# Kernel tuning notes

Measured on AMD Instinct MI355X. Metric: run time of the kernel, lower is better.

Reference implementation:

```python
import jax, jax.numpy as jnp
import numpy as np

EMBED_DIM = 1024
NUM_HEADS = 16
D_K = EMBED_DIM // NUM_HEADS  # 64 quantum wires per head


def setup_inputs() -> dict:
    key = jax.random.key(0)
    k1, k2, k3 = jax.random.split(key, 3)
    x = jax.random.normal(k1, (8, 2048, EMBED_DIM), dtype=jnp.float32)
    # single shared projection weight (source creates ONE nn.Linear used for q,k,v and out)
    W = jax.random.normal(k2, (EMBED_DIM, EMBED_DIM), dtype=jnp.float32) * 0.02
    # trainable RY angles, one per wire, shared across tokens and heads
    theta = jax.random.normal(k3, (D_K,), dtype=jnp.float32)
    return {"x": x, "W": W, "theta": theta}


def _quantum_project(h, theta):
    # h: [B, S, E] -> per-head wires [B, S, H, d_k]
    # Circuit per wire i: |0> -> RX(h_i) -> RY(theta_i) -> <Z>
    # Product state closed form: <Z> = cos(theta_i) * cos(h_i)
    B, S, E = h.shape
    hw = h.reshape(B, S, NUM_HEADS, D_K)
    return jnp.cos(theta) * jnp.cos(hw)  # [B, S, H, d_k]


def reference(x, W, theta):
    # one Linear (no bias) shared by q, k, v -> identical projections
    proj = x @ W.T  # [B, S, E]
    qq = _quantum_project(proj, theta)  # == k_q == v_q, [B, S, H, d_k]
    # scores attend heads-vs-heads per token (faithful to source matmul on dims -2,-1)
    scores = jnp.einsum('bshd,bsgd->bshg', qq, qq) / np.sqrt(D_K).astype(np.float32)
    attn = jax.nn.softmax(scores, axis=-1)  # dropout omitted (eval)
    out = jnp.einsum('bshg,bsgd->bshd', attn, qq)  # [B, S, H, d_k]
    B, S = x.shape[0], x.shape[1]
    out = out.reshape(B, S, EMBED_DIM) @ W.T  # output projection with same shared linear
    return out
```

## Files before the change

### kernel.cpp

```cpp
#include <hip/hip_runtime.h>
#include <hip/hip_bf16.h>
#include <stdint.h>

#define NB    8
#define NS    2048
#define NE    1024
#define NH    16
#define NDK   64
#define MTOK  (NB*NS)

typedef __attribute__((ext_vector_type(8))) short bf16x8;
typedef __attribute__((ext_vector_type(4))) float f32x4;

__device__ __forceinline__ ushort f2bf(float f) {
  uint32_t u = __float_as_uint(f);
  u += 0x7FFFu + ((u >> 16) & 1u);
  return (ushort)(u >> 16);
}

__device__ __forceinline__ void gload16(const void* g, void* l) {
  __builtin_amdgcn_global_load_lds(
      (const __attribute__((address_space(1))) void*)g,
      (__attribute__((address_space(3))) void*)l, 16, 0, 0);
}

__global__ __launch_bounds__(256) void cvt_bf16(const float* __restrict__ in,
                                                ushort* __restrict__ out, int n4) {
  int stride = gridDim.x * blockDim.x;
  for (int j = blockIdx.x * blockDim.x + threadIdx.x; j < n4; j += stride) {
    float4 v = ((const float4*)in)[j];
    ushort4 o;
    o.x = f2bf(v.x); o.y = f2bf(v.y); o.z = f2bf(v.z); o.w = f2bf(v.w);
    ((ushort4*)out)[j] = o;
  }
}

#define GM 256
#define GN 256
#define GK 64
#define KC 1024
#define NKT (KC / GK)

template<int EPI>
__global__ __launch_bounds__(512, 2) void gemm256(const ushort* __restrict__ A,
                                                  const ushort* __restrict__ Bm,
                                                  float* __restrict__ Cf,
                                                  ushort* __restrict__ Cq,
                                                  const float* __restrict__ theta,
                                                  int M, int N, int K) {
  __shared__ ushort As[2][GM * GK];
  __shared__ ushort Bs[2][GN * GK];

  const int tid  = threadIdx.x;
  const int wid  = tid >> 6;
  const int lane = tid & 63;
  const int wr   = wid >> 2;
  const int wc   = wid & 3;
  const int fr   = lane & 15;
  const int ks   = lane >> 4;

  int b  = blockIdx.x;
  int wg = ((b & 7) << 5) | (b >> 3);
  int br = wg >> 2, bc = wg & 3;

  const ushort* Abase = A  + (size_t)(br * GM) * KC;
  const ushort* Bbase = Bm + (size_t)(bc * GN) * KC;

  const int srow = lane >> 3;
  const int sch8 = ((lane & 7) ^ srow) * 8;

  const int sA0 = ((0 + ks) ^ (fr & 7)) * 8;
  const int sA1 = ((4 + ks) ^ (fr & 7)) * 8;

  f32x4 zero = {0.f, 0.f, 0.f, 0.f};
  f32x4 acc[8][4];
#pragma unroll
  for (int mi = 0; mi < 8; ++mi)
#pragma unroll
    for (int ni = 0; ni < 4; ++ni) acc[mi][ni] = zero;

  auto stA = [&](int buf, int mh, int kt) {
#pragma unroll
    for (int j = 0; j < 2; ++j) {
      int rl = mh * 128 + j * 64 + wid * 8;
      gload16(Abase + (size_t)(rl + srow) * KC + kt * GK + sch8,
              &As[buf][rl * GK]);
    }
  };
  auto stB = [&](int buf, int mh, int kt) {
#pragma unroll
    for (int j = 0; j < 2; ++j) {
      int rl = mh * 128 + j * 64 + wid * 8;
      gload16(Bbase + (size_t)(rl + srow) * KC + kt * GK + sch8,
              &Bs[buf][rl * GK]);
    }
  };

  stB(0, 0, 0); stB(0, 1, 0); stA(0, 0, 0); stA(0, 1, 0);
  asm volatile("s_waitcnt vmcnt(2)" ::: "memory");
  __builtin_amdgcn_s_barrier();

  int cur = 0;
  for (int t = 0; t < NKT; ++t) {
    const ushort* Ac = As[cur];
    const ushort* Bc = Bs[cur];
    const int nb = cur ^ 1;
    const bool pf = (t + 1 < NKT);
    bf16x8 af[4], bv[4];

#pragma unroll
    for (int mi = 0; mi < 4; ++mi)
      af[mi] = *(const bf16x8*)&Ac[(mi * 32 + wr * 16 + fr) * GK + sA0];
#pragma unroll
    for (int ni = 0; ni < 4; ++ni)
      bv[ni] = *(const bf16x8*)&Bc[(ni * 64 + wc * 16 + fr) * GK + sA0];
    if (pf) { stB(nb, 0, t + 1); stB(nb, 1, t + 1); stA(nb, 0, t + 1); stA(nb, 1, t + 1); }
    __builtin_amdgcn_sched_barrier(0);
    __builtin_amdgcn_s_setprio(1);
#pragma unroll
    for (int mi = 0; mi < 4; ++mi)
#pragma unroll
      for (int ni = 0; ni < 4; ++ni)
        acc[mi][ni] = __builtin_amdgcn_mfma_f32_16x16x32_bf16(af[mi], bv[ni], acc[mi][ni], 0, 0, 0);
    __builtin_amdgcn_s_setprio(0);
    __builtin_amdgcn_sched_barrier(0);
    if (pf) asm volatile("s_waitcnt vmcnt(8)" ::: "memory");
    else    asm volatile("s_waitcnt vmcnt(0)" ::: "memory");
    __builtin_amdgcn_s_barrier();

#pragma unroll
    for (int mi = 0; mi < 4; ++mi)
      af[mi] = *(const bf16x8*)&Ac[((mi + 4) * 32 + wr * 16 + fr) * GK + sA0];
    __builtin_amdgcn_sched_barrier(0);
    __builtin_amdgcn_s_setprio(1);
#pragma unroll
    for (int mi = 0; mi < 4; ++mi)
#pragma unroll
      for (int ni = 0; ni < 4; ++ni)
        acc[mi + 4][ni] = __builtin_amdgcn_mfma_f32_16x16x32_bf16(af[mi], bv[ni], acc[mi + 4][ni], 0, 0, 0);
    __builtin_amdgcn_s_setprio(0);
    __builtin_amdgcn_sched_barrier(0);

#pragma unroll
    for (int mi = 0; mi < 4; ++mi)
      af[mi] = *(const bf16x8*)&Ac[(mi * 32 + wr * 16 + fr) * GK + sA1];
#pragma unroll
    for (int ni = 0; ni < 4; ++ni)
      bv[ni] = *(const bf16x8*)&Bc[(ni * 64 + wc * 16 + fr) * GK + sA1];
    __builtin_amdgcn_sched_barrier(0);
    __builtin_amdgcn_s_setprio(1);
#pragma unroll
    for (int mi = 0; mi < 4; ++mi)
#pragma unroll
      for (int ni = 0; ni < 4; ++ni)
        acc[mi][ni] = __builtin_amdgcn_mfma_f32_16x16x32_bf16(af[mi], bv[ni], acc[mi][ni], 0, 0, 0);
    __builtin_amdgcn_s_setprio(0);
    __builtin_amdgcn_sched_barrier(0);

#pragma unroll
    for (int mi = 0; mi < 4; ++mi)
      af[mi] = *(const bf16x8*)&Ac[((mi + 4) * 32 + wr * 16 + fr) * GK + sA1];
    __builtin_amdgcn_sched_barrier(0);
    __builtin_amdgcn_s_setprio(1);
#pragma unroll
    for (int mi = 0; mi < 4; ++mi)
#pragma unroll
      for (int ni = 0; ni < 4; ++ni)
        acc[mi + 4][ni] = __builtin_amdgcn_mfma_f32_16x16x32_bf16(af[mi], bv[ni], acc[mi + 4][ni], 0, 0, 0);
    __builtin_amdgcn_s_setprio(0);
    __builtin_amdgcn_sched_barrier(0);
    if (pf) asm volatile("s_waitcnt vmcnt(2)" ::: "memory");
    __builtin_amdgcn_s_barrier();

    cur ^= 1;
  }

  const int colL = wc * 16 + fr;
  float ct = 0.f;
  if (EPI == 1) ct = __cosf(theta[colL]);
#pragma unroll
  for (int mi = 0; mi < 8; ++mi) {
    int row0 = br * GM + mi * 32 + wr * 16 + ks * 4;
#pragma unroll
    for (int ni = 0; ni < 4; ++ni) {
      size_t cbase = (size_t)row0 * N + bc * GN + ni * 64 + colL;
#pragma unroll
      for (int i = 0; i < 4; ++i) {
        if (EPI == 1)
          Cq[cbase + (size_t)i * N] = f2bf(ct * __cosf(acc[mi][ni][i]));
        else
          Cf[cbase + (size_t)i * N] = acc[mi][ni][i];
      }
    }
  }
}

__global__ __launch_bounds__(256) void attn_quantum(const ushort* __restrict__ qqb,
                                                    ushort* __restrict__ aout) {
  __shared__ ushort T[4][64 * 32];
  int tid = threadIdx.x;
  int wv  = tid >> 6, l = tid & 63;
  size_t tok = (size_t)blockIdx.x * 4 + wv;
  const ushort* src = qqb + tok * NE;
  ushort* Tw = T[wv];

  int h  = l & 15;
  int kb = l >> 4;

  bf16x8 f0 = *(const bf16x8*)(src + h * 64 + kb * 8);
  bf16x8 f1 = *(const bf16x8*)(src + h * 64 + kb * 8 + 32);

#pragma unroll
  for (int jj = 0; jj < 8; ++jj) {
    int d0 = kb * 8 + jj;
    int d1 = d0 + 32;
    Tw[d0 * 32 + (((h >> 3) ^ ((d0 >> 3) & 3)) << 3) + (h & 7)] = (ushort)f0[jj];
    Tw[d1 * 32 + (((h >> 3) ^ ((d1 >> 3) & 3)) << 3) + (h & 7)] = (ushort)f1[jj];
  }

  f32x4 sa = {0.f, 0.f, 0.f, 0.f};
  sa = __builtin_amdgcn_mfma_f32_16x16x32_bf16(f0, f0, sa, 0, 0, 0);
  sa = __builtin_amdgcn_mfma_f32_16x16x32_bf16(f1, f1, sa, 0, 0, 0);

  float s[4];
#pragma unroll
  for (int i = 0; i < 4; ++i) s[i] = sa[i] * 0.125f;

  float mx = fmaxf(fmaxf(s[0], s[1]), fmaxf(s[2], s[3]));
  mx = fmaxf(mx, __shfl_xor(mx, 16));
  mx = fmaxf(mx, __shfl_xor(mx, 32));
  float e[4], sum = 0.f;
#pragma unroll
  for (int i = 0; i < 4; ++i) { e[i] = __expf(s[i] - mx); sum += e[i]; }
  sum += __shfl_xor(sum, 16);
  sum += __shfl_xor(sum, 32);
  float inv = 1.f / sum;
#pragma unroll
  for (int i = 0; i < 4; ++i) e[i] *= inv;

  int s1 = h + (kb & 1) * 32;
  float q1[4], q2[4];
#pragma unroll
  for (int i = 0; i < 4; ++i) {
    q1[i] = __shfl(e[i], s1);
    q2[i] = __shfl(e[i], s1 + 16);
  }
  bool live = (kb < 2);
  bf16x8 pa;
#pragma unroll
  for (int i = 0; i < 4; ++i) {
    pa[i]     = live ? (short)f2bf(q1[i]) : (short)0;
    pa[4 + i] = live ? (short)f2bf(q2[i]) : (short)0;
  }

  __syncthreads();

  f32x4 o[4];
#pragma unroll
  for (int c = 0; c < 4; ++c) {
    int r = c * 16 + h;
    int slot = (kb & 1) ^ ((r >> 3) & 3);
    bf16x8 bfrag = *(const bf16x8*)&Tw[r * 32 + slot * 8];
    f32x4 z = {0.f, 0.f, 0.f, 0.f};
    o[c] = __builtin_amdgcn_mfma_f32_16x16x32_bf16(pa, bfrag, z, 0, 0, 0);
  }

  ushort* dst = aout + tok * NE;
#pragma unroll
  for (int c = 0; c < 4; ++c)
#pragma unroll
    for (int i = 0; i < 4; ++i)
      dst[(kb * 4 + i) * NDK + c * 16 + h] = f2bf(o[c][i]);
}

extern "C" void kernel_launch(void* const* d_in, const int* in_sizes, int n_in,
                              void* d_out, int out_size, void* d_ws, size_t ws_size,
                              hipStream_t stream) {
  const float* x     = (const float*)d_in[0];
  const float* W     = (const float*)d_in[1];
  const float* theta = (const float*)d_in[2];
  float* out = (float*)d_out;

  char* ws = (char*)d_ws;
  ushort* xb   = (ushort*)ws;
  ushort* Wb   = (ushort*)(ws + (size_t)MTOK * NE * 2);
  ushort* qqb  = (ushort*)(ws + (size_t)MTOK * NE * 2 + (size_t)NE * NE * 2);
  ushort* aout = xb;

  cvt_bf16<<<1024, 256, 0, stream>>>(x, xb, MTOK * NE / 4);
  cvt_bf16<<<256, 256, 0, stream>>>(W, Wb, NE * NE / 4);

  int nwg = (MTOK / GM) * (NE / GN);
  gemm256<1><<<nwg, 512, 0, stream>>>(xb, Wb, nullptr, qqb, theta, MTOK, NE, NE);

  attn_quantum<<<MTOK / 4, 256, 0, stream>>>(qqb, aout);

  gemm256<0><<<nwg, 512, 0, stream>>>(aout, Wb, out, nullptr, nullptr, MTOK, NE, NE);
}
```

Measured before the change: 109.9 us.

## Fuse fp32-to-bf16 conversion of x into first projection GEMM

Removes the standalone conversion pass over x and adds a dedicated GEMM that reads fp32 x directly, converts it in registers, and writes bf16 tiles into swizzled LDS with a two-stage register prefetch. The tile is 128x256 with one workgroup per CU, and the cos(theta)*cos(h) epilogue is applied directly. This saves a full write and re-read of the 32MB bf16 copy of x. The trade-off is more global traffic per A tile, since fp32 is twice the bytes, and lower occupancy, which may make the GEMM's latency hiding worse.

```diff
diff --git a/kernel.cpp b/kernel.cpp
--- a/kernel.cpp
+++ b/kernel.cpp
@@ -35,11 +35,178 @@
   }
 }
 
+#define KC 1024
+#define NKT 16
+
+#define QM 128
+#define QN 256
+#define QK 64
+
+#define LOADAQ(kt, AR)                                                        \
+  do {                                                                        \
+    _Pragma("unroll")                                                         \
+    for (int j = 0; j < 4; ++j)                                               \
+      AR[j] = X4[(size_t)(br * QM + ar_r) * 256 + (kt) * 16 + c4 * 4 + j];    \
+  } while (0)
+
+#define WRITEAQ(buf, AR)                                                      \
+  do {                                                                        \
+    bf16x8 v0, v1;                                                            \
+    v0[0] = (short)f2bf(AR[0].x); v0[1] = (short)f2bf(AR[0].y);               \
+    v0[2] = (short)f2bf(AR[0].z); v0[3] = (short)f2bf(AR[0].w);               \
+    v0[4] = (short)f2bf(AR[1].x); v0[5] = (short)f2bf(AR[1].y);               \
+    v0[6] = (short)f2bf(AR[1].z); v0[7] = (short)f2bf(AR[1].w);               \
+    v1[0] = (short)f2bf(AR[2].x); v1[1] = (short)f2bf(AR[2].y);               \
+    v1[2] = (short)f2bf(AR[2].z); v1[3] = (short)f2bf(AR[2].w);               \
+    v1[4] = (short)f2bf(AR[3].x); v1[5] = (short)f2bf(AR[3].y);               \
+    v1[6] = (short)f2bf(AR[3].z); v1[7] = (short)f2bf(AR[3].w);               \
+    *(bf16x8*)&As[buf][ar_r * QK + wrs0] = v0;                                \
+    *(bf16x8*)&As[buf][ar_r * QK + wrs1] = v1;                                \
+  } while (0)
+
+#define QMFMA(MOFF)                                                           \
+  __builtin_amdgcn_sched_barrier(0);                                          \
+  __builtin_amdgcn_s_setprio(1);                                              \
+  _Pragma("unroll")                                                           \
+  for (int mi = 0; mi < 2; ++mi)                                              \
+    _Pragma("unroll")                                                         \
+    for (int ni = 0; ni < 4; ++ni)                                            \
+      acc[mi + (MOFF)][ni] = __builtin_amdgcn_mfma_f32_16x16x32_bf16(         \
+          af[mi], bv[ni], acc[mi + (MOFF)][ni], 0, 0, 0);                     \
+  __builtin_amdgcn_s_setprio(0);                                              \
+  __builtin_amdgcn_sched_barrier(0);
+
+#define BODYQ(T, ARL, ARW)                                                    \
+  {                                                                           \
+    const int t = (T);                                                        \
+    const ushort* Ac = As[cur];                                               \
+    const ushort* Bc = Bs[cur];                                               \
+    const int nb = cur ^ 1;                                                   \
+    const bool pf  = (t + 1 < NKT);                                           \
+    const bool pf2 = (t + 2 < NKT);                                           \
+    bf16x8 af[2], bv[4];                                                      \
+                      \
+    _Pragma("unroll")                                                         \
+    for (int mi = 0; mi < 2; ++mi)                                            \
+      af[mi] = *(const bf16x8*)&Ac[(wr * 64 + mi * 16 + fr) * QK + sA0];      \
+    _Pragma("unroll")                                                         \
+    for (int ni = 0; ni < 4; ++ni)                                            \
+      bv[ni] = *(const bf16x8*)&Bc[(ni * 64 + wc * 16 + fr) * QK + sA0];      \
+    if (pf) { stB(nb, 0, t + 1); stB(nb, 1, t + 1); }                         \
+    if (pf2) LOADAQ(t + 2, ARL);                                              \
+    QMFMA(0)                                                                  \
+                                      \
+    _Pragma("unroll")                                                         \
+    for (int mi = 0; mi < 2; ++mi)                                            \
+      af[mi] = *(const bf16x8*)&Ac[(wr * 64 + (mi + 2) * 16 + fr) * QK + sA0];\
+    QMFMA(2)                                                                  \
+                                                        \
+    _Pragma("unroll")                                                         \
+    for (int mi = 0; mi < 2; ++mi)                                            \
+      af[mi] = *(const bf16x8*)&Ac[(wr * 64 + mi * 16 + fr) * QK + sA1];      \
+    _Pragma("unroll")                                                         \
+    for (int ni = 0; ni < 4; ++ni)                                            \
+      bv[ni] = *(const bf16x8*)&Bc[(ni * 64 + wc * 16 + fr) * QK + sA1];      \
+    QMFMA(0)                                                                  \
+                                  \
+    _Pragma("unroll")                                                         \
+    for (int mi = 0; mi < 2; ++mi)                                            \
+      af[mi] = *(const bf16x8*)&Ac[(wr * 64 + (mi + 2) * 16 + fr) * QK + sA1];\
+    QMFMA(2)                                                                  \
+    if (pf) {                                                                 \
+      if (pf2) asm volatile("s_waitcnt vmcnt(4)" ::: "memory");               \
+      else     asm volatile("s_waitcnt vmcnt(0)" ::: "memory");               \
+      WRITEAQ(nb, ARW);                                                       \
+      asm volatile("s_waitcnt lgkmcnt(0)" ::: "memory");                      \
+    }                                                                         \
+    __builtin_amdgcn_s_barrier();                                             \
+    cur ^= 1;                                                                 \
+  }
+
+__global__ __launch_bounds__(512, 1) void gemm_xq(const float* __restrict__ X,
+                                                  const ushort* __restrict__ Bm,
+                                                  ushort* __restrict__ Cq,
+                                                  const float* __restrict__ theta) {
+  __shared__ ushort As[2][QM * QK];
+  __shared__ ushort Bs[2][QN * QK];
+
+  const int tid  = threadIdx.x;
+  const int wid  = tid >> 6;
+  const int lane = tid & 63;
+  const int wr   = wid >> 2;
+  const int wc   = wid & 3;
+  const int fr   = lane & 15;
+  const int ks   = lane >> 4;
+
+  int b  = blockIdx.x;
+  int wg = ((b & 7) << 6) | (b >> 3);
+  int br = wg >> 2, bc = wg & 3;
+
+  const ushort* Bbase = Bm + (size_t)(bc * QN) * KC;
+  const float4* X4    = (const float4*)X;
+
+  const int srow = lane >> 3;
+  const int sch8 = ((lane & 7) ^ srow) * 8;
+
+  const int ar_r = wid * 16 + (lane >> 2);
+  const int c4   = lane & 3;
+  const int wrs0 = ((2 * c4)     ^ (ar_r & 7)) * 8;
+  const int wrs1 = ((2 * c4 + 1) ^ (ar_r & 7)) * 8;
+
+  const int sA0 = ((0 + ks) ^ (fr & 7)) * 8;
+  const int sA1 = ((4 + ks) ^ (fr & 7)) * 8;
+
+  f32x4 zero = {0.f, 0.f, 0.f, 0.f};
+  f32x4 acc[4][4];
+#pragma unroll
+  for (int mi = 0; mi < 4; ++mi)
+#pragma unroll
+    for (int ni = 0; ni < 4; ++ni) acc[mi][ni] = zero;
+
+  auto stB = [&](int buf, int mh, int kt) {
+#pragma unroll
+    for (int j = 0; j < 2; ++j) {
+      int rl = mh * 128 + j * 64 + wid * 8;
+      gload16(Bbase + (size_t)(rl + srow) * KC + kt * QK + sch8,
+              &Bs[buf][rl * QK]);
+    }
+  };
+
+  float4 arP[4], arQ[4];
+
+  LOADAQ(0, arP);
+  asm volatile("s_waitcnt vmcnt(0)" ::: "memory");
+  WRITEAQ(0, arP);
+  stB(0, 0, 0); stB(0, 1, 0);
+  LOADAQ(1, arQ);
+  asm volatile("s_waitcnt vmcnt(4)" ::: "memory");
+  asm volatile("s_waitcnt lgkmcnt(0)" ::: "memory");
+  __builtin_amdgcn_s_barrier();
+
+  int cur = 0;
+  for (int t2 = 0; t2 < NKT; t2 += 2) {
+    BODYQ(t2,     arP, arQ)
+    BODYQ(t2 + 1, arQ, arP)
+  }
+
+  const int colL = wc * 16 + fr;
+  float ct = __cosf(theta[colL]);
+#pragma unroll
+  for (int mi = 0; mi < 4; ++mi) {
+    int row0 = br * QM + wr * 64 + mi * 16 + ks * 4;
+#pragma unroll
+    for (int ni = 0; ni < 4; ++ni) {
+      size_t cbase = (size_t)row0 * NE + bc * QN + ni * 64 + colL;
+#pragma unroll
+      for (int i = 0; i < 4; ++i)
+        Cq[cbase + (size_t)i * NE] = f2bf(ct * __cosf(acc[mi][ni][i]));
+    }
+  }
+}
+
 #define GM 256
 #define GN 256
 #define GK 64
-#define KC 1024
-#define NKT (KC / GK)
 
 template<int EPI>
 __global__ __launch_bounds__(512, 2) void gemm256(const ushort* __restrict__ A,
@@ -282,18 +449,15 @@
   float* out = (float*)d_out;
 
   char* ws = (char*)d_ws;
-  ushort* xb   = (ushort*)ws;
-  ushort* Wb   = (ushort*)(ws + (size_t)MTOK * NE * 2);
-  ushort* qqb  = (ushort*)(ws + (size_t)MTOK * NE * 2 + (size_t)NE * NE * 2);
-  ushort* aout = xb;
-
-  cvt_bf16<<<1024, 256, 0, stream>>>(x, xb, MTOK * NE / 4);
+  ushort* Wb   = (ushort*)ws;
+  ushort* qqb  = (ushort*)(ws + (size_t)NE * NE * 2);
+  ushort* aout = (ushort*)(ws + (size_t)NE * NE * 2 + (size_t)MTOK * NE * 2);
+
   cvt_bf16<<<256, 256, 0, stream>>>(W, Wb, NE * NE / 4);
 
-  int nwg = (MTOK / GM) * (NE / GN);
-  gemm256<1><<<nwg, 512, 0, stream>>>(xb, Wb, nullptr, qqb, theta, MTOK, NE, NE);
+  gemm_xq<<<(MTOK / QM) * (NE / QN), 512, 0, stream>>>(x, Wb, qqb, theta);
 
   attn_quantum<<<MTOK / 4, 256, 0, stream>>>(qqb, aout);
 
-  gemm256<0><<<nwg, 512, 0, stream>>>(aout, Wb, out, nullptr, nullptr, MTOK, NE, NE);
-}
+  gemm256<0><<<(MTOK / GM) * (NE / GN), 512, 0, stream>>>(aout, Wb, out, nullptr, nullptr, MTOK, NE, NE);
+}
```

New measurement: 114.4 us. 4.2% more time.
